# Kernel tuning notes

Measured on AMD Instinct MI355X. Metric: run time of the kernel, lower is better.

Reference implementation:

```python
import jax, jax.numpy as jnp
import numpy as np

NUM_HIDDENS = 512
NUM_HEADS = 4
B, S = 4, 2048


def setup_inputs() -> dict:
    key = jax.random.key(0)
    ks = jax.random.split(key, 10)
    H = NUM_HIDDENS
    scale = 1.0 / np.sqrt(H)
    return {
        "queries": jax.random.normal(ks[0], (B, S, H), jnp.float32),
        "keys": jax.random.normal(ks[1], (B, S, H), jnp.float32),
        "values": jax.random.normal(ks[2], (B, S, H), jnp.float32),
        "attention_mask": jax.random.randint(ks[3], (B, S), 0, 2).astype(bool),
        "Wq": jax.random.normal(ks[4], (H, H), jnp.float32) * scale,
        "bq": jnp.zeros((H,), jnp.float32),
        "Wk": jax.random.normal(ks[5], (H, H), jnp.float32) * scale,
        "bk": jnp.zeros((H,), jnp.float32),
        "Wv": jax.random.normal(ks[6], (H, H), jnp.float32) * scale,
        "bv": jnp.zeros((H,), jnp.float32),
    }


def reference(queries, keys, values, attention_mask, Wq, bq, Wk, bk, Wv, bv):
    B_, S_, H = queries.shape
    nh = NUM_HEADS
    dh = H // nh

    # QKV projections with ReLU (as in the original Sequential(Linear, ReLU))
    q = jax.nn.relu(jnp.einsum("bsh,oh->bso", queries, Wq) + bq)
    k = jax.nn.relu(jnp.einsum("bsh,oh->bso", keys, Wk) + bk)
    v = jax.nn.relu(jnp.einsum("bsh,oh->bso", values, Wv) + bv)

    # chunk along last dim + stack dim=1  ==  reshape [B,S,nh,dh] -> [B,nh,S,dh]
    qs = q.reshape(B_, S_, nh, dh).transpose(0, 2, 1, 3)
    ks_ = k.reshape(B_, S_, nh, dh).transpose(0, 2, 1, 3)
    vs = v.reshape(B_, S_, nh, dh).transpose(0, 2, 1, 3)

    # scores [B, nh, S, S]
    score = jnp.einsum("bhqd,bhkd->bhqk", qs, ks_) / jnp.sqrt(jnp.float32(dh))

    # 'enc' mask: [B,S] -> [B,1,S,1], fills entire QUERY rows (faithful quirk)
    row_mask = attention_mask[:, None, :, None]
    score = jnp.where(row_mask, jnp.float32(-1e9), score)

    attn = jax.nn.softmax(score, axis=-1)
    a = jnp.einsum("bhqk,bhkd->bhqd", attn, vs)  # [B, nh, S, dh]

    # faithful quirk: permute(0,1,3,2) then reshape to (B, S, H)
    a = jnp.transpose(a, (0, 1, 3, 2)).reshape(B_, S_, H)
    return a + queries
```

## Files before the change

kernel.cpp:

```cpp
#include <hip/hip_runtime.h>
#include <hip/hip_bf16.h>

typedef __attribute__((ext_vector_type(8)))  __bf16 bf16x8;
typedef __attribute__((ext_vector_type(4)))  __bf16 bf16x4;
typedef __attribute__((ext_vector_type(2)))  __bf16 bf16x2;
typedef __attribute__((ext_vector_type(4)))  float  f32x4;
typedef __attribute__((ext_vector_type(16))) float  f32x16;

#define MFMA16(a,b,c) __builtin_amdgcn_mfma_f32_16x16x32_bf16((a),(b),(c),0,0,0)
#define MFMA32(a,b,c) __builtin_amdgcn_mfma_f32_32x32x16_bf16((a),(b),(c),0,0,0)

__device__ inline void gload_lds16(const __bf16* g, __bf16* l) {
  __builtin_amdgcn_global_load_lds(
      (const __attribute__((address_space(1))) void*)g,
      (__attribute__((address_space(3))) void*)l, 16, 0, 0);
}

__global__ __launch_bounds__(256) void convert_kernel(
    const float* __restrict__ Xq, const float* __restrict__ Xk,
    const float* __restrict__ Xv, const float* __restrict__ Wq,
    const float* __restrict__ Wk, const float* __restrict__ Wv,
    __bf16* __restrict__ dXq, __bf16* __restrict__ dXk, __bf16* __restrict__ dXv,
    __bf16* __restrict__ dWq, __bf16* __restrict__ dWk, __bf16* __restrict__ dWv)
{
  const int which = blockIdx.y;
  const float* src;
  __bf16* dst;
  size_t idx;
  if (blockIdx.x < 4096) {
    src = which == 0 ? Xq : which == 1 ? Xk : Xv;
    dst = which == 0 ? dXq : which == 1 ? dXk : dXv;
    idx = (size_t)blockIdx.x * 256 + threadIdx.x;
  } else {
    src = which == 0 ? Wq : which == 1 ? Wk : Wv;
    dst = which == 0 ? dWq : which == 1 ? dWk : dWv;
    idx = (size_t)(blockIdx.x - 4096) * 256 + threadIdx.x;
  }
  float4 v = *(const float4*)&src[idx * 4];
  bf16x4 o;
  o[0] = (__bf16)v.x; o[1] = (__bf16)v.y; o[2] = (__bf16)v.z; o[3] = (__bf16)v.w;
  *(bf16x4*)&dst[idx * 4] = o;
}

__global__ __launch_bounds__(256, 2) void gemm_kernel(
    const __bf16* __restrict__ Xqb, const __bf16* __restrict__ Xkb,
    const __bf16* __restrict__ Xvb, const __bf16* __restrict__ Wqb,
    const __bf16* __restrict__ Wkb, const __bf16* __restrict__ Wvb,
    const float* __restrict__ bq, const float* __restrict__ bk,
    const float* __restrict__ bv, const int* __restrict__ mask,
    __bf16* __restrict__ dq, __bf16* __restrict__ dk, __bf16* __restrict__ dv)
{
  const int which = blockIdx.z;
  const __bf16* X   = which == 0 ? Xqb : which == 1 ? Xkb : Xvb;
  const __bf16* W   = which == 0 ? Wqb : which == 1 ? Wkb : Wvb;
  const float* bias = which == 0 ? bq : which == 1 ? bk : bv;
  __bf16* dst       = which == 0 ? dq : which == 1 ? dk : dv;
  const float oscale = which == 0 ? 0.12751744710339033f : 1.0f;
  const int mode = (which == 2);

  __shared__ __align__(16) __bf16 Al[2][128 * 64];
  __shared__ __align__(16) __bf16 Bl[2][128 * 64];

  const int tid  = threadIdx.x;
  const int lane = tid & 63;
  const int w    = tid >> 6;
  const int wr = w >> 1, wc = w & 1;
  const int mbase = blockIdx.x * 128;
  const int nbase = blockIdx.y * 128;
  const int arow = lane & 15;
  const int hi   = lane >> 4;

  f32x4 acc[4][4] = {};

  auto stage = [&](int buf, int k0) {
#pragma unroll
    for (int i = 0; i < 4; ++i) {
      int ob = w * 4096 + i * 1024;
      int o  = ob + lane * 16;
      int r  = o >> 7;
      int s  = ((o >> 4) & 7) ^ (r & 7);
      gload_lds16(X + (size_t)(mbase + r) * 512 + k0 + s * 8, &Al[buf][ob >> 1]);
    }
#pragma unroll
    for (int i = 0; i < 4; ++i) {
      int ob = w * 4096 + i * 1024;
      int o  = ob + lane * 16;
      int r  = o >> 7;
      int s  = ((o >> 4) & 7) ^ (r & 7);
      gload_lds16(W + (size_t)(nbase + r) * 512 + k0 + s * 8, &Bl[buf][ob >> 1]);
    }
  };

  stage(0, 0);

  for (int t = 0; t < 8; ++t) {
    const int cur = t & 1;
    if (t < 7) {
      stage(cur ^ 1, (t + 1) * 64);
      asm volatile("s_waitcnt vmcnt(8)" ::: "memory");
    } else {
      asm volatile("s_waitcnt vmcnt(0)" ::: "memory");
    }
    __builtin_amdgcn_s_barrier();

    __builtin_amdgcn_s_setprio(1);
#pragma unroll
    for (int kk = 0; kk < 2; ++kk) {
      bf16x8 af[4], bfr[4];
#pragma unroll
      for (int m = 0; m < 4; ++m) {
        int row = wr * 64 + m * 16 + arow;
        int sl  = ((kk * 4 + hi) ^ (row & 7)) * 8;
        af[m] = *(bf16x8*)&Al[cur][row * 64 + sl];
      }
#pragma unroll
      for (int n = 0; n < 4; ++n) {
        int row = wc * 64 + n * 16 + arow;
        int sl  = ((kk * 4 + hi) ^ (row & 7)) * 8;
        bfr[n] = *(bf16x8*)&Bl[cur][row * 64 + sl];
      }
#pragma unroll
      for (int m = 0; m < 4; ++m)
#pragma unroll
        for (int n = 0; n < 4; ++n)
          acc[m][n] = MFMA16(af[m], bfr[n], acc[m][n]);
    }
    __builtin_amdgcn_s_setprio(0);

    __builtin_amdgcn_s_barrier();
  }

#pragma unroll
  for (int n = 0; n < 4; ++n) {
    int col = nbase + wc * 64 + n * 16 + arow;
    float bsv = bias[col];
    int h = col >> 7, d = col & 127;
#pragma unroll
    for (int m = 0; m < 4; ++m) {
      int row0 = mbase + wr * 64 + m * 16 + hi * 4;
#pragma unroll
      for (int r = 0; r < 4; ++r) {
        float v = acc[m][n][r] + bsv;
        v = (v > 0.0f ? v : 0.0f) * oscale;
        int mm = row0 + r;
        int b = mm >> 11, s = mm & 2047;
        if (which == 0 && mask[b * 2048 + s] != 0) v = 0.0f;
        if (mode == 0)
          dst[((size_t)(b * 4 + h) * 2048 + s) * 128 + d] = (__bf16)v;
        else
          dst[((size_t)(b * 4 + h) * 128 + d) * 2048 + s] = (__bf16)v;
      }
    }
  }
}

__global__ __launch_bounds__(256, 2) void attn_kernel(
    const __bf16* __restrict__ qh, const __bf16* __restrict__ kh,
    const __bf16* __restrict__ vt, const float* __restrict__ queries,
    float* __restrict__ out)
{
  __shared__ __align__(16) __bf16 Kl[2][64 * 128];
  __shared__ __align__(16) __bf16 Vl[2][128 * 64];

  const int tid  = threadIdx.x;
  const int lane = tid & 63;
  const int w    = tid >> 6;
  const int qw   = w & 1;
  const int kw   = w >> 1;
  const int r5   = lane & 31;
  const int hi32 = lane >> 5;

  const int blk = blockIdx.x;
  const int xcd = blk & 7;
  const int idx = blk >> 3;
  const int bh  = xcd * 2 + (idx & 1);
  const int qt  = idx >> 1;
  const int b = bh >> 2, h = bh & 3;
  const int qbase = qt * 64 + qw * 32;

  const __bf16* qptr = qh + (size_t)bh * 2048 * 128;
  const __bf16* kptr = kh + (size_t)bh * 2048 * 128;
  const __bf16* vptr = vt + (size_t)bh * 128 * 2048;

  bf16x8 qf[8];
#pragma unroll
  for (int ds = 0; ds < 8; ++ds)
    qf[ds] = *(const bf16x8*)&qptr[(size_t)(qbase + r5) * 128 + ds * 16 + hi32 * 8];

  float l_st = 0.f;
  f32x16 oacc[4] = {};

  auto stageK = [&](int buf, int kv0) {
#pragma unroll
    for (int i = 0; i < 4; ++i) {
      int ob = i * 4096 + w * 1024;
      int o  = ob + lane * 16;
      int r  = o >> 8;
      int s  = ((o >> 4) & 15) ^ (r & 7);
      gload_lds16(kptr + (size_t)(kv0 + r) * 128 + s * 8, &Kl[buf][ob >> 1]);
    }
  };
  auto stageV = [&](int buf, int kv0) {
#pragma unroll
    for (int i = 0; i < 4; ++i) {
      int ob = i * 4096 + w * 1024;
      int o  = ob + lane * 16;
      int r  = o >> 7;
      int s  = ((o >> 4) & 7) ^ (r & 7);
      gload_lds16(vptr + (size_t)r * 2048 + kv0 + s * 8, &Vl[buf][ob >> 1]);
    }
  };

  stageK(0, 0);
  stageV(0, 0);

  for (int t = 0; t < 32; ++t) {
    const int cur = t & 1;
    if (t < 31) {
      stageK(cur ^ 1, (t + 1) * 64);
      stageV(cur ^ 1, (t + 1) * 64);
      asm volatile("s_waitcnt vmcnt(8)" ::: "memory");
    } else {
      asm volatile("s_waitcnt vmcnt(0)" ::: "memory");
    }
    __builtin_amdgcn_s_barrier();

    f32x16 sacc = {};
    __builtin_amdgcn_s_setprio(1);
#pragma unroll
    for (int ds = 0; ds < 8; ++ds) {
      int row = kw * 32 + r5;
      int sl  = ((ds * 2 + hi32) ^ (row & 7)) * 8;
      bf16x8 kf = *(bf16x8*)&Kl[cur][row * 128 + sl];
      sacc = MFMA32(kf, qf[ds], sacc);
    }
    __builtin_amdgcn_s_setprio(0);

    float rsum = 0.f;
#pragma unroll
    for (int r = 0; r < 16; ++r) {
      float p = __builtin_amdgcn_exp2f(sacc[r]);
      sacc[r] = p;
      rsum += p;
    }
    l_st += rsum;

    unsigned pk[8];
#pragma unroll
    for (int g = 0; g < 8; ++g) {
      bf16x2 tp;
      tp[0] = (__bf16)sacc[2 * g];
      tp[1] = (__bf16)sacc[2 * g + 1];
      pk[g] = __builtin_bit_cast(unsigned, tp);
    }
    bf16x8 pf[2];
#pragma unroll
    for (int s = 0; s < 2; ++s) {
      unsigned a0 = pk[4 * s + 0], a1 = pk[4 * s + 1];
      unsigned b0 = pk[4 * s + 2], b1 = pk[4 * s + 3];
      asm("v_permlane32_swap_b32 %0, %1" : "+v"(a0), "+v"(b0));
      asm("v_permlane32_swap_b32 %0, %1" : "+v"(a1), "+v"(b1));
      union { unsigned u[4]; bf16x8 v; } pu;
      pu.u[0] = a0; pu.u[1] = a1; pu.u[2] = b0; pu.u[3] = b1;
      pf[s] = pu.v;
    }

    __builtin_amdgcn_s_setprio(1);
#pragma unroll
    for (int dblk = 0; dblk < 4; ++dblk) {
#pragma unroll
      for (int s = 0; s < 2; ++s) {
        int row = dblk * 32 + r5;
        int s0  = kw * 4 + s * 2 + hi32;
        int sl  = (s0 ^ (row & 7)) * 8;
        bf16x8 vf = *(bf16x8*)&Vl[cur][row * 64 + sl];
        oacc[dblk] = MFMA32(vf, pf[s], oacc[dblk]);
      }
    }
    __builtin_amdgcn_s_setprio(0);

    __builtin_amdgcn_s_barrier();
  }

  float l_tot = l_st + __shfl_xor(l_st, 32);

  __syncthreads();
  float* Ll = (float*)&Kl[0][0];
  float* Ob = Ll + 64;

  if (kw == 1) {
    if (hi32 == 0) Ll[qw * 32 + r5] = l_tot;
    float* dst = Ob + (size_t)(qw * 64 + lane) * 68;
#pragma unroll
    for (int dblk = 0; dblk < 4; ++dblk)
      *(f32x16*)(dst + dblk * 16) = oacc[dblk];
  }
  __syncthreads();

  if (kw == 0) {
    float l1 = Ll[qw * 32 + r5];
    float inv = 1.0f / (l_tot + l1);
    const float* src = Ob + (size_t)(qw * 64 + lane) * 68;

    const int qhi = qt >> 3;
    const int col = (qt & 7) * 64 + qw * 32 + r5;
#pragma unroll
    for (int dblk = 0; dblk < 4; ++dblk) {
      f32x16 o1 = *(const f32x16*)(src + dblk * 16);
#pragma unroll
      for (int r = 0; r < 16; ++r) {
        int d = dblk * 32 + (r & 3) + 8 * (r >> 2) + 4 * hi32;
        int srow = h * 512 + d * 4 + qhi;
        size_t o = ((size_t)b * 2048 + srow) * 512 + col;
        out[o] = (oacc[dblk][r] + o1[r]) * inv + queries[o];
      }
    }
  }
}

extern "C" void kernel_launch(void* const* d_in, const int* in_sizes, int n_in,
                              void* d_out, int out_size, void* d_ws, size_t ws_size,
                              hipStream_t stream) {
  const float* queries = (const float*)d_in[0];
  const float* keys    = (const float*)d_in[1];
  const float* values  = (const float*)d_in[2];
  const int*   mask    = (const int*)d_in[3];
  const float* Wq = (const float*)d_in[4];
  const float* bq = (const float*)d_in[5];
  const float* Wk = (const float*)d_in[6];
  const float* bk = (const float*)d_in[7];
  const float* Wv = (const float*)d_in[8];
  const float* bv = (const float*)d_in[9];
  float* out = (float*)d_out;

  const size_t perX = (size_t)8192 * 512;
  const size_t perW = (size_t)512 * 512;
  __bf16* qhp = (__bf16*)d_ws;
  __bf16* khp = qhp + perX;
  __bf16* vtp = khp + perX;
  __bf16* Xqb = vtp + perX;
  __bf16* Xkb = Xqb + perX;
  __bf16* Xvb = Xkb + perX;
  __bf16* Wqb = Xvb + perX;
  __bf16* Wkb = Wqb + perW;
  __bf16* Wvb = Wkb + perW;

  convert_kernel<<<dim3(4352, 3), dim3(256), 0, stream>>>(
      queries, keys, values, Wq, Wk, Wv, Xqb, Xkb, Xvb, Wqb, Wkb, Wvb);

  gemm_kernel<<<dim3(64, 4, 3), dim3(256), 0, stream>>>(
      Xqb, Xkb, Xvb, Wqb, Wkb, Wvb, bq, bk, bv, mask, qhp, khp, vtp);

  attn_kernel<<<dim3(512), dim3(256), 0, stream>>>(qhp, khp, vtp, queries, out);
}
```

Before: 91.17 us.

## Fuse fp32-to-bf16 conversion into GEMM staging and load V directly from global

Drops the separate conversion kernel. The GEMM now loads fp32 inputs and weights into registers, converts them to bf16 and writes them to swizzled LDS with a register-prefetch double buffer, which removes one launch and the bf16 round-trip through memory. In the attention kernel, V fragments are read straight from global memory into registers instead of being staged through LDS, and the row-sum uses a tree reduction. The attention change trades LDS traffic for uncoalesced-ish direct global loads and more registers, and the GEMM loses its async global-to-LDS loads.

```diff
diff --git a/kernel.cpp b/kernel.cpp
--- a/kernel.cpp
+++ b/kernel.cpp
@@ -16,43 +16,17 @@
       (__attribute__((address_space(3))) void*)l, 16, 0, 0);
 }
 
-__global__ __launch_bounds__(256) void convert_kernel(
+__global__ __launch_bounds__(256, 2) void gemm_kernel(
     const float* __restrict__ Xq, const float* __restrict__ Xk,
     const float* __restrict__ Xv, const float* __restrict__ Wq,
     const float* __restrict__ Wk, const float* __restrict__ Wv,
-    __bf16* __restrict__ dXq, __bf16* __restrict__ dXk, __bf16* __restrict__ dXv,
-    __bf16* __restrict__ dWq, __bf16* __restrict__ dWk, __bf16* __restrict__ dWv)
-{
-  const int which = blockIdx.y;
-  const float* src;
-  __bf16* dst;
-  size_t idx;
-  if (blockIdx.x < 4096) {
-    src = which == 0 ? Xq : which == 1 ? Xk : Xv;
-    dst = which == 0 ? dXq : which == 1 ? dXk : dXv;
-    idx = (size_t)blockIdx.x * 256 + threadIdx.x;
-  } else {
-    src = which == 0 ? Wq : which == 1 ? Wk : Wv;
-    dst = which == 0 ? dWq : which == 1 ? dWk : dWv;
-    idx = (size_t)(blockIdx.x - 4096) * 256 + threadIdx.x;
-  }
-  float4 v = *(const float4*)&src[idx * 4];
-  bf16x4 o;
-  o[0] = (__bf16)v.x; o[1] = (__bf16)v.y; o[2] = (__bf16)v.z; o[3] = (__bf16)v.w;
-  *(bf16x4*)&dst[idx * 4] = o;
-}
-
-__global__ __launch_bounds__(256, 2) void gemm_kernel(
-    const __bf16* __restrict__ Xqb, const __bf16* __restrict__ Xkb,
-    const __bf16* __restrict__ Xvb, const __bf16* __restrict__ Wqb,
-    const __bf16* __restrict__ Wkb, const __bf16* __restrict__ Wvb,
     const float* __restrict__ bq, const float* __restrict__ bk,
     const float* __restrict__ bv, const int* __restrict__ mask,
     __bf16* __restrict__ dq, __bf16* __restrict__ dk, __bf16* __restrict__ dv)
 {
   const int which = blockIdx.z;
-  const __bf16* X   = which == 0 ? Xqb : which == 1 ? Xkb : Xvb;
-  const __bf16* W   = which == 0 ? Wqb : which == 1 ? Wkb : Wvb;
+  const float* X    = which == 0 ? Xq : which == 1 ? Xk : Xv;
+  const float* W    = which == 0 ? Wq : which == 1 ? Wk : Wv;
   const float* bias = which == 0 ? bq : which == 1 ? bk : bv;
   __bf16* dst       = which == 0 ? dq : which == 1 ? dk : dv;
   const float oscale = which == 0 ? 0.12751744710339033f : 1.0f;
@@ -71,37 +45,41 @@
   const int hi   = lane >> 4;
 
   f32x4 acc[4][4] = {};
-
-  auto stage = [&](int buf, int k0) {
-#pragma unroll
-    for (int i = 0; i < 4; ++i) {
-      int ob = w * 4096 + i * 1024;
-      int o  = ob + lane * 16;
-      int r  = o >> 7;
-      int s  = ((o >> 4) & 7) ^ (r & 7);
-      gload_lds16(X + (size_t)(mbase + r) * 512 + k0 + s * 8, &Al[buf][ob >> 1]);
-    }
-#pragma unroll
-    for (int i = 0; i < 4; ++i) {
-      int ob = w * 4096 + i * 1024;
-      int o  = ob + lane * 16;
-      int r  = o >> 7;
-      int s  = ((o >> 4) & 7) ^ (r & 7);
-      gload_lds16(W + (size_t)(nbase + r) * 512 + k0 + s * 8, &Bl[buf][ob >> 1]);
+  float4 ar[8], br[8];
+
+  auto issue = [&](int k0) {
+#pragma unroll
+    for (int i = 0; i < 8; ++i) {
+      int idx = tid + i * 256;
+      int r = idx >> 4, c = (idx & 15) * 4;
+      ar[i] = *(const float4*)&X[(size_t)(mbase + r) * 512 + k0 + c];
+      br[i] = *(const float4*)&W[(size_t)(nbase + r) * 512 + k0 + c];
     }
   };
-
-  stage(0, 0);
+  auto commit = [&](int buf) {
+#pragma unroll
+    for (int i = 0; i < 8; ++i) {
+      int idx = tid + i * 256;
+      int r = idx >> 4, c4 = idx & 15;
+      int slot = c4 >> 1, half = c4 & 1;
+      int addr = r * 64 + (slot ^ (r & 7)) * 8 + half * 4;
+      bf16x4 av, bv2;
+      av[0] = (__bf16)ar[i].x; av[1] = (__bf16)ar[i].y;
+      av[2] = (__bf16)ar[i].z; av[3] = (__bf16)ar[i].w;
+      bv2[0] = (__bf16)br[i].x; bv2[1] = (__bf16)br[i].y;
+      bv2[2] = (__bf16)br[i].z; bv2[3] = (__bf16)br[i].w;
+      *(bf16x4*)&Al[buf][addr] = av;
+      *(bf16x4*)&Bl[buf][addr] = bv2;
+    }
+  };
+
+  issue(0);
+  commit(0);
 
   for (int t = 0; t < 8; ++t) {
     const int cur = t & 1;
-    if (t < 7) {
-      stage(cur ^ 1, (t + 1) * 64);
-      asm volatile("s_waitcnt vmcnt(8)" ::: "memory");
-    } else {
-      asm volatile("s_waitcnt vmcnt(0)" ::: "memory");
-    }
-    __builtin_amdgcn_s_barrier();
+    if (t < 7) issue((t + 1) * 64);
+    __syncthreads();
 
     __builtin_amdgcn_s_setprio(1);
 #pragma unroll
@@ -127,7 +105,7 @@
     }
     __builtin_amdgcn_s_setprio(0);
 
-    __builtin_amdgcn_s_barrier();
+    if (t < 7) commit(cur ^ 1);
   }
 
 #pragma unroll
@@ -160,7 +138,7 @@
     float* __restrict__ out)
 {
   __shared__ __align__(16) __bf16 Kl[2][64 * 128];
-  __shared__ __align__(16) __bf16 Vl[2][128 * 64];
+  __shared__ float Mbuf[64 + 128 * 68];
 
   const int tid  = threadIdx.x;
   const int lane = tid & 63;
@@ -200,29 +178,29 @@
       gload_lds16(kptr + (size_t)(kv0 + r) * 128 + s * 8, &Kl[buf][ob >> 1]);
     }
   };
-  auto stageV = [&](int buf, int kv0) {
-#pragma unroll
-    for (int i = 0; i < 4; ++i) {
-      int ob = i * 4096 + w * 1024;
-      int o  = ob + lane * 16;
-      int r  = o >> 7;
-      int s  = ((o >> 4) & 7) ^ (r & 7);
-      gload_lds16(vptr + (size_t)r * 2048 + kv0 + s * 8, &Vl[buf][ob >> 1]);
-    }
-  };
 
   stageK(0, 0);
-  stageV(0, 0);
 
   for (int t = 0; t < 32; ++t) {
     const int cur = t & 1;
     if (t < 31) {
       stageK(cur ^ 1, (t + 1) * 64);
-      stageV(cur ^ 1, (t + 1) * 64);
-      asm volatile("s_waitcnt vmcnt(8)" ::: "memory");
+      asm volatile("s_waitcnt vmcnt(4)" ::: "memory");
     } else {
       asm volatile("s_waitcnt vmcnt(0)" ::: "memory");
     }
+
+    bf16x8 vf[4][2];
+#pragma unroll
+    for (int dblk = 0; dblk < 4; ++dblk)
+#pragma unroll
+      for (int s = 0; s < 2; ++s) {
+        int row  = dblk * 32 + r5;
+        int slot = kw * 4 + s * 2 + hi32;
+        vf[dblk][s] =
+            *(const bf16x8*)&vptr[(size_t)row * 2048 + t * 64 + slot * 8];
+      }
+
     __builtin_amdgcn_s_barrier();
 
     f32x16 sacc = {};
@@ -236,14 +214,18 @@
     }
     __builtin_amdgcn_s_setprio(0);
 
-    float rsum = 0.f;
+    float ps[16];
 #pragma unroll
     for (int r = 0; r < 16; ++r) {
-      float p = __builtin_amdgcn_exp2f(sacc[r]);
-      sacc[r] = p;
-      rsum += p;
-    }
-    l_st += rsum;
+      ps[r] = __builtin_amdgcn_exp2f(sacc[r]);
+      sacc[r] = ps[r];
+    }
+#pragma unroll
+    for (int st = 1; st < 16; st <<= 1)
+#pragma unroll
+      for (int r = 0; r < 16; r += 2 * st)
+        ps[r] += ps[r + st];
+    l_st += ps[0];
 
     unsigned pk[8];
 #pragma unroll
@@ -267,16 +249,10 @@
 
     __builtin_amdgcn_s_setprio(1);
 #pragma unroll
-    for (int dblk = 0; dblk < 4; ++dblk) {
-#pragma unroll
-      for (int s = 0; s < 2; ++s) {
-        int row = dblk * 32 + r5;
-        int s0  = kw * 4 + s * 2 + hi32;
-        int sl  = (s0 ^ (row & 7)) * 8;
-        bf16x8 vf = *(bf16x8*)&Vl[cur][row * 64 + sl];
-        oacc[dblk] = MFMA32(vf, pf[s], oacc[dblk]);
-      }
-    }
+    for (int dblk = 0; dblk < 4; ++dblk)
+#pragma unroll
+      for (int s = 0; s < 2; ++s)
+        oacc[dblk] = MFMA32(vf[dblk][s], pf[s], oacc[dblk]);
     __builtin_amdgcn_s_setprio(0);
 
     __builtin_amdgcn_s_barrier();
@@ -285,8 +261,8 @@
   float l_tot = l_st + __shfl_xor(l_st, 32);
 
   __syncthreads();
-  float* Ll = (float*)&Kl[0][0];
-  float* Ob = Ll + 64;
+  float* Ll = Mbuf;
+  float* Ob = Mbuf + 64;
 
   if (kw == 1) {
     if (hi32 == 0) Ll[qw * 32 + r5] = l_tot;
@@ -334,22 +310,12 @@
   float* out = (float*)d_out;
 
   const size_t perX = (size_t)8192 * 512;
-  const size_t perW = (size_t)512 * 512;
   __bf16* qhp = (__bf16*)d_ws;
   __bf16* khp = qhp + perX;
   __bf16* vtp = khp + perX;
-  __bf16* Xqb = vtp + perX;
-  __bf16* Xkb = Xqb + perX;
-  __bf16* Xvb = Xkb + perX;
-  __bf16* Wqb = Xvb + perX;
-  __bf16* Wkb = Wqb + perW;
-  __bf16* Wvb = Wkb + perW;
-
-  convert_kernel<<<dim3(4352, 3), dim3(256), 0, stream>>>(
-      queries, keys, values, Wq, Wk, Wv, Xqb, Xkb, Xvb, Wqb, Wkb, Wvb);
 
   gemm_kernel<<<dim3(64, 4, 3), dim3(256), 0, stream>>>(
-      Xqb, Xkb, Xvb, Wqb, Wkb, Wvb, bq, bk, bv, mask, qhp, khp, vtp);
+      queries, keys, values, Wq, Wk, Wv, bq, bk, bv, mask, qhp, khp, vtp);
 
   attn_kernel<<<dim3(512), dim3(256), 0, stream>>>(qhp, khp, vtp, queries, out);
 }
```

Result: slower. 111.0 us (+21.7%).
